# Kernel optimization log

Hardware: AMD Instinct MI355X
Metric: run time of the kernel (lower is better)

The kernel has to match this reference:

```python
import jax, jax.numpy as jnp
import numpy as np
from jax import lax

B, L = 2048, 2048
CIN, CONV, D, NCLS = 1, 128, 1024, 1000
E, H, K = 6, 2 * 1024, 2  # num_experts, expert hidden, top-k


def setup_inputs() -> dict:
    key = jax.random.key(0)
    ks = jax.random.split(key, 16)
    s = lambda *sh: 0.02
    return {
        "x": jax.random.normal(ks[0], (B, L), jnp.float32),
        "conv1_w": jax.random.normal(ks[1], (CONV, CIN, 5), jnp.float32) * 0.1,
        "conv1_b": jnp.zeros((CONV,), jnp.float32),
        "conv2_w": jax.random.normal(ks[2], (CONV, CONV, 5), jnp.float32) * 0.05,
        "conv2_b": jnp.zeros((CONV,), jnp.float32),
        "proj_w": jax.random.normal(ks[3], (D, CONV), jnp.float32) * 0.05,
        "proj_b": jnp.zeros((D,), jnp.float32),
        "router_w": jax.random.normal(ks[4], (E, D), jnp.float32) * 0.02,
        "router_b": jnp.zeros((E,), jnp.float32),
        "exp_w1": jax.random.normal(ks[5], (E, H, D), jnp.float32) * 0.02,
        "exp_b1": jnp.zeros((E, H), jnp.float32),
        "exp_w2": jax.random.normal(ks[6], (E, D, H), jnp.float32) * 0.02,
        "exp_b2": jnp.zeros((E, D), jnp.float32),
        "cls_w": jax.random.normal(ks[7], (NCLS, D), jnp.float32) * 0.02,
        "cls_b": jnp.zeros((NCLS,), jnp.float32),
    }


def _conv1d(x, w, b):
    # x: [B, C, L]; torch Conv1d(k=5, stride=2, pad=2)
    y = lax.conv_general_dilated(x, w, window_strides=(2,), padding=[(2, 2)],
                                 dimension_numbers=("NCH", "OIH", "NCH"))
    return y + b[None, :, None]


def reference(x, conv1_w, conv1_b, conv2_w, conv2_b, proj_w, proj_b,
              router_w, router_b, exp_w1, exp_b1, exp_w2, exp_b2, cls_w, cls_b):
    h = x[:, None, :]                               # [B,1,L]
    h = jax.nn.relu(_conv1d(h, conv1_w, conv1_b))   # [B,CONV,L/2]
    h = jax.nn.relu(_conv1d(h, conv2_w, conv2_b))   # [B,CONV,L/4]
    h = h.mean(axis=-1)                             # [B,CONV]
    h = h @ proj_w.T + proj_b                       # [B,D]

    # Top-2 router
    probs = jax.nn.softmax(h @ router_w.T + router_b, axis=-1)  # [B,E]
    top_vals, top_idx = lax.top_k(probs, K)                     # [B,2]
    # per-token per-expert combine weights (exact same math as masked loop)
    combine = (jax.nn.one_hot(top_idx[:, 0], E, dtype=h.dtype) * top_vals[:, 0:1]
               + jax.nn.one_hot(top_idx[:, 1], E, dtype=h.dtype) * top_vals[:, 1:2])  # [B,E]

    # all-expert FFN, then masked combine (equivalent to gather/scatter dispatch)
    hid = jax.nn.relu(jnp.einsum("bd,ehd->beh", h, exp_w1) + exp_b1)  # [B,E,H]
    eo = jnp.einsum("beh,edh->bed", hid, exp_w2) + exp_b2             # [B,E,D]
    moe = jnp.einsum("be,bed->bd", combine, eo)                       # [B,D]

    return moe @ cls_w.T + cls_b                                      # [B,NCLS]
```

## Files before the change

### kernel.cpp

```cpp
#include <hip/hip_runtime.h>
#include <hip/hip_bf16.h>
#include <hip/hip_fp16.h>
#include <stdint.h>

#define BB 2048
#define LL 2048
#define CV 128
#define DD 1024
#define NC 1000
#define EE 6
#define HH 2048

typedef __bf16 bf16_t;
typedef _Float16 f16_t;
typedef __attribute__((ext_vector_type(8))) __bf16 bf16x8;
typedef __attribute__((ext_vector_type(8))) _Float16 f16x8;
typedef __attribute__((ext_vector_type(4))) _Float16 f16x4;
typedef __attribute__((ext_vector_type(4))) float f32x4;

__device__ __forceinline__ void gload_lds16(const void* g, void* l)
{
    __builtin_amdgcn_global_load_lds(
        (const __attribute__((address_space(1))) unsigned int*)g,
        (__attribute__((address_space(3))) unsigned int*)l, 16, 0, 0);
}

__global__ void k_prep_w2(const float* __restrict__ w2, bf16_t* __restrict__ wsw)
{
    int idx = blockIdx.x * 256 + threadIdx.x;
    if (idx >= 5 * 128 * 128) return;
    int kk = idx % 5;
    int t2 = idx / 5;
    int ci = t2 & 127;
    int co = t2 >> 7;
    float v = w2[idx];
    bf16_t h = (bf16_t)v;
    bf16_t l = (bf16_t)(v - (float)h);
    int cb = ci >> 5, j = ci & 31;
    int t  = cb * 5 + kk;
    int si = (co * 32 + j) ^ ((co & 7) << 3);
    wsw[(size_t)t * 8192 + si]        = h;
    wsw[(size_t)t * 8192 + 4096 + si] = l;
}

__global__ void k_prep_exp(const float* __restrict__ ew1, const float* __restrict__ ew2,
                           const float* __restrict__ cw,  f16_t* __restrict__ ew1h,
                           f16_t* __restrict__ ew2h, f16_t* __restrict__ clsh)
{
    const size_t n1 = (size_t)EE * HH * DD / 4;
    const size_t n2 = n1 + (size_t)EE * DD * HH / 4;
    const size_t n3 = n2 + (size_t)NC * DD / 4;
    size_t i4 = (size_t)blockIdx.x * 256 + threadIdx.x;
    if (i4 >= n3) return;
    const float* src; f16_t* dst; size_t off;
    if (i4 < n1)      { src = ew1; dst = ew1h; off = i4; }
    else if (i4 < n2) { src = ew2; dst = ew2h; off = i4 - n1; }
    else              { src = cw;  dst = clsh; off = i4 - n2; }
    float4 v = reinterpret_cast<const float4*>(src)[off];
    f16x4 r;
    r[0] = (f16_t)v.x; r[1] = (f16_t)v.y; r[2] = (f16_t)v.z; r[3] = (f16_t)v.w;
    reinterpret_cast<f16x4*>(dst)[off] = r;
}

__launch_bounds__(256, 2)
__global__ void k_conv(const float* __restrict__ x,  const float* __restrict__ w1,
                       const float* __restrict__ b1, const bf16_t* __restrict__ wsw,
                       const float* __restrict__ b2, float* __restrict__ hbar)
{
    __shared__ __align__(16) float w1s[640];
    __shared__ __align__(16) float b1s[128];
    __shared__ __align__(16) float b2s[128];
    __shared__ __align__(16) short h1s[2][260 * 32];
    __shared__ __align__(16) short wlds[2][8192];

    const int tid  = threadIdx.x;
    const int b    = blockIdx.x;
    const int lane = tid & 63;
    const int wid  = tid >> 6;
    const int l15  = lane & 15, lg = lane >> 4;
    const int wm   = wid >> 1,  wn = wid & 1;
    const int jo   = tid & 3;
    const int rg   = tid >> 2;

    short* wflat = &wlds[0][0];

    for (int i = tid; i < 640; i += 256) w1s[i] = w1[i];
    if (tid < 128) { b1s[tid] = b1[tid]; b2s[tid] = b2[tid]; }

    {
        const bf16_t* src = wsw + (size_t)(wid * 4) * 512 + lane * 8;
        short* dst = wflat + (wid * 4) * 512;
#pragma unroll
        for (int o = 0; o < 4; ++o)
            gload_lds16(src + o * 512, dst + o * 512);
    }
    __syncthreads();

    const float* xrow = x + (size_t)b * LL;

    float racc[4][4];
#pragma unroll
    for (int m = 0; m < 4; ++m)
#pragma unroll
        for (int r = 0; r < 4; ++r) racc[m][r] = 0.f;

    for (int c = 0; c < 4; ++c) {
        const int t1base = 256 * c - 2;

        f32x4 acc[4][4];
#pragma unroll
        for (int m = 0; m < 4; ++m)
#pragma unroll
            for (int n = 0; n < 4; ++n)
#pragma unroll
                for (int r = 0; r < 4; ++r) acc[m][n][r] = 0.f;

        for (int cb = 0; cb < 4; ++cb) {
            const int ci0 = cb * 32 + jo * 8;
            float wf[40], br8[8];
#pragma unroll
            for (int q = 0; q < 10; ++q)
                *reinterpret_cast<float4*>(&wf[q * 4]) =
                    *reinterpret_cast<const float4*>(&w1s[ci0 * 5 + q * 4]);
            *reinterpret_cast<float4*>(&br8[0]) = *reinterpret_cast<const float4*>(&b1s[ci0]);
            *reinterpret_cast<float4*>(&br8[4]) = *reinterpret_cast<const float4*>(&b1s[ci0 + 4]);

#pragma unroll
            for (int it = 0; it < 5; ++it) {
                int r = rg + it * 64;
                if (it < 4 || r < 260) {
                    int t1 = t1base + r;
                    bool valid = (unsigned)t1 < 1024u;
                    float xv[5];
#pragma unroll
                    for (int kk = 0; kk < 5; ++kk) {
                        int xg = 2 * t1 - 2 + kk;
                        xv[kk] = (valid && (unsigned)xg < 2048u) ? xrow[xg] : 0.f;
                    }
                    bf16x8 hv, lv;
#pragma unroll
                    for (int u = 0; u < 8; ++u) {
                        float v = 0.f;
                        if (valid) {
                            v = br8[u];
#pragma unroll
                            for (int kk = 0; kk < 5; ++kk) v += wf[u * 5 + kk] * xv[kk];
                            v = fmaxf(v, 0.f);
                        }
                        bf16_t h = (bf16_t)v;
                        hv[u] = h;
                        lv[u] = (bf16_t)(v - (float)h);
                    }
                    int si = (r * 32 + jo * 8) ^ (((r >> 1) & 7) << 3);
                    *reinterpret_cast<bf16x8*>(&h1s[0][si]) = hv;
                    *reinterpret_cast<bf16x8*>(&h1s[1][si]) = lv;
                }
            }
            __syncthreads();

            for (int k = 0; k < 5; ++k) {
                const int t  = cb * 5 + k;
                const int tn = (t + 1) % 20;
                {
                    const bf16_t* src = wsw + (size_t)tn * 8192 + (wid * 4) * 512 + lane * 8;
                    short* dst = wflat + (tn & 1) * 8192 + (wid * 4) * 512;
#pragma unroll
                    for (int o = 0; o < 4; ++o)
                        gload_lds16(src + o * 512, dst + o * 512);
                }
                const short* wp = wflat + (t & 1) * 8192;
                bf16x8 ah[4], al[4];
#pragma unroll
                for (int m = 0; m < 4; ++m) {
                    int co_l = wm * 64 + m * 16 + l15;
                    int si = (co_l * 32 + lg * 8) ^ ((l15 & 7) << 3);
                    ah[m] = *reinterpret_cast<const bf16x8*>(wp + si);
                    al[m] = *reinterpret_cast<const bf16x8*>(wp + 4096 + si);
                }
                bf16x8 bh[4], bl[4];
#pragma unroll
                for (int n = 0; n < 4; ++n) {
                    int r = 2 * (wn * 64 + n * 16 + l15) + k;
                    int si = (r * 32 + lg * 8) ^ (((r >> 1) & 7) << 3);
                    bh[n] = *reinterpret_cast<const bf16x8*>(&h1s[0][si]);
                    bl[n] = *reinterpret_cast<const bf16x8*>(&h1s[1][si]);
                }
#pragma unroll
                for (int m = 0; m < 4; ++m)
#pragma unroll
                    for (int n = 0; n < 4; ++n) {
                        acc[m][n] = __builtin_amdgcn_mfma_f32_16x16x32_bf16(ah[m], bh[n], acc[m][n], 0, 0, 0);
                        acc[m][n] = __builtin_amdgcn_mfma_f32_16x16x32_bf16(ah[m], bl[n], acc[m][n], 0, 0, 0);
                        acc[m][n] = __builtin_amdgcn_mfma_f32_16x16x32_bf16(al[m], bh[n], acc[m][n], 0, 0, 0);
                    }
                __syncthreads();
            }
        }
#pragma unroll
        for (int m = 0; m < 4; ++m)
#pragma unroll
            for (int r = 0; r < 4; ++r) {
                int co = wm * 64 + m * 16 + lg * 4 + r;
                float bias = b2s[co];
                float s = 0.f;
#pragma unroll
                for (int n = 0; n < 4; ++n) s += fmaxf(acc[m][n][r] + bias, 0.f);
                racc[m][r] += s;
            }
    }

    asm volatile("s_waitcnt vmcnt(0)" ::: "memory");
    __syncthreads();

#pragma unroll
    for (int m = 0; m < 4; ++m)
#pragma unroll
        for (int r = 0; r < 4; ++r) {
            float v = racc[m][r];
            v += __shfl_xor(v, 1);
            v += __shfl_xor(v, 2);
            v += __shfl_xor(v, 4);
            v += __shfl_xor(v, 8);
            racc[m][r] = v;
        }
    float* red = (float*)wflat;
    if (l15 == 0) {
#pragma unroll
        for (int m = 0; m < 4; ++m)
#pragma unroll
            for (int r = 0; r < 4; ++r)
                red[wid * 64 + m * 16 + lg * 4 + r] = racc[m][r];
    }
    __syncthreads();
    if (tid < 128) {
        int wm2 = tid >> 6, loc = tid & 63;
        float s = red[(wm2 * 2 + 0) * 64 + loc] + red[(wm2 * 2 + 1) * 64 + loc];
        hbar[(size_t)b * 128 + tid] = s * (1.f / 512.f);
    }
}

__launch_bounds__(256)
__global__ void k_proj(const float* __restrict__ hbar, const float* __restrict__ pw,
                       const float* __restrict__ pb, float* __restrict__ h)
{
    __shared__ float hbs[64 * 128];
    const int tid = threadIdx.x;
    const int b0 = blockIdx.x * 64, d0 = blockIdx.y * 64;
    for (int i = tid * 4; i < 64 * 128; i += 1024)
        *reinterpret_cast<float4*>(&hbs[i]) =
            *reinterpret_cast<const float4*>(&hbar[(size_t)b0 * 128 + i]);
    __syncthreads();
    const int tx = tid & 15, ty = tid >> 4;
    float acc[4][4];
#pragma unroll
    for (int i = 0; i < 4; ++i)
#pragma unroll
        for (int j = 0; j < 4; ++j) acc[i][j] = 0.f;
    const float* pwr[4];
#pragma unroll
    for (int j = 0; j < 4; ++j) pwr[j] = pw + (size_t)(d0 + tx * 4 + j) * 128;
    for (int k = 0; k < 128; k += 4) {
        float4 wv[4], av[4];
#pragma unroll
        for (int j = 0; j < 4; ++j) wv[j] = *reinterpret_cast<const float4*>(pwr[j] + k);
#pragma unroll
        for (int i = 0; i < 4; ++i) av[i] = *reinterpret_cast<const float4*>(&hbs[(ty * 4 + i) * 128 + k]);
#pragma unroll
        for (int i = 0; i < 4; ++i)
#pragma unroll
            for (int j = 0; j < 4; ++j)
                acc[i][j] += av[i].x * wv[j].x + av[i].y * wv[j].y +
                             av[i].z * wv[j].z + av[i].w * wv[j].w;
    }
#pragma unroll
    for (int i = 0; i < 4; ++i) {
        int bb = b0 + ty * 4 + i;
#pragma unroll
        for (int j = 0; j < 4; ++j) {
            int d = d0 + tx * 4 + j;
            h[(size_t)bb * DD + d] = acc[i][j] + pb[d];
        }
    }
}

__launch_bounds__(256)
__global__ void k_router(const float* __restrict__ h, const float* __restrict__ rw,
                         const float* __restrict__ rb, float* __restrict__ comb,
                         int2* __restrict__ top)
{
    const int lane = threadIdx.x & 63;
    const int b = blockIdx.x * 4 + (threadIdx.x >> 6);
    float part[6] = {0.f, 0.f, 0.f, 0.f, 0.f, 0.f};
    for (int j = 0; j < 16; ++j) {
        int d = j * 64 + lane;
        float hv = h[(size_t)b * DD + d];
#pragma unroll
        for (int e = 0; e < 6; ++e) part[e] += rw[e * DD + d] * hv;
    }
#pragma unroll
    for (int e = 0; e < 6; ++e) {
        float v = part[e];
        for (int off = 32; off > 0; off >>= 1) v += __shfl_xor(v, off);
        part[e] = v;
    }
    if (lane == 0) {
        float lgt[6];
#pragma unroll
        for (int e = 0; e < 6; ++e) lgt[e] = part[e] + rb[e];
        int i1 = 0;
#pragma unroll
        for (int e = 1; e < 6; ++e) if (lgt[e] > lgt[i1]) i1 = e;
        int i2 = -1;
#pragma unroll
        for (int e = 0; e < 6; ++e)
            if (e != i1 && (i2 < 0 || lgt[e] > lgt[i2])) i2 = e;
        float mx = lgt[i1], s = 0.f, ex[6];
#pragma unroll
        for (int e = 0; e < 6; ++e) { ex[e] = expf(lgt[e] - mx); s += ex[e]; }
        float inv = 1.f / s;
#pragma unroll
        for (int e = 0; e < 6; ++e) comb[b * 8 + e] = 0.f;
        comb[b * 8 + 6] = 0.f; comb[b * 8 + 7] = 0.f;
        comb[b * 8 + i1] = ex[i1] * inv;
        comb[b * 8 + i2] = ex[i2] * inv;
        top[b] = make_int2(i1, i2);
    }
}

__global__ void k_index(const int2* __restrict__ top, int* __restrict__ meta,
                        int* __restrict__ idxg)
{
    __shared__ int wsum[4];
    const int tid = threadIdx.x, lane = tid & 63, wid = tid >> 6;
    int2 tk[8];
#pragma unroll
    for (int j = 0; j < 8; ++j) tk[j] = top[tid * 8 + j];
    int off_run = 0;
    for (int e = 0; e < 6; ++e) {
        int m[8], c = 0;
#pragma unroll
        for (int j = 0; j < 8; ++j) { m[j] = (tk[j].x == e || tk[j].y == e) ? 1 : 0; c += m[j]; }
        int v = c;
        for (int d = 1; d < 64; d <<= 1) { int u = __shfl_up(v, d); if (lane >= d) v += u; }
        if (lane == 63) wsum[wid] = v;
        __syncthreads();
        int wbase = 0;
#pragma unroll
        for (int w = 0; w < 4; ++w) if (w < wid) wbase += wsum[w];
        int total = wsum[0] + wsum[1] + wsum[2] + wsum[3];
        int p = off_run + wbase + (v - c);
#pragma unroll
        for (int j = 0; j < 8; ++j) if (m[j]) idxg[p++] = tid * 8 + j;
        if (tid == 0) { meta[e] = total; meta[8 + e] = off_run; }
        off_run += total;
        __syncthreads();
    }
    if (tid == 0) meta[14] = off_run;
}

__device__ inline f16x8 cvt8(const float4 a, const float4 b)
{
    f16x8 r;
    r[0] = (f16_t)a.x; r[1] = (f16_t)a.y; r[2] = (f16_t)a.z; r[3] = (f16_t)a.w;
    r[4] = (f16_t)b.x; r[5] = (f16_t)b.y; r[6] = (f16_t)b.z; r[7] = (f16_t)b.w;
    return r;
}

template<int EPI, int NFRAG>
__launch_bounds__(256, 3)
__global__ void k_moe(const float* __restrict__ hsrc, const f16_t* __restrict__ hidg,
                      const f16_t* __restrict__ eog, const float* __restrict__ Bp,
                      const f16_t* __restrict__ Bh, const float* __restrict__ bias,
                      f16_t* __restrict__ outH, f16_t* __restrict__ eogW,
                      float* __restrict__ outF, const float* __restrict__ comb,
                      const int2* __restrict__ top, const int* __restrict__ meta,
                      const int* __restrict__ idxg, int N, int K, int NCLIP)
{
    constexpr int BN = NFRAG * 32;
    __shared__ f16_t As[128 * 72];
    __shared__ f16_t Bs[BN * 72];
    const int tid = threadIdx.x;
    const int e  = blockIdx.z;
    const int m0 = blockIdx.x * 128, n0 = blockIdx.y * BN;
    int cnt = 1 << 30, off = 0;
    if (EPI != 3) {
        cnt = meta[e]; off = meta[8 + e];
        if (m0 >= cnt) return;
    }
    const int lane = tid & 63, wid = tid >> 6;
    const int l15 = lane & 15, lg = lane >> 4;
    const int wm = wid >> 1, wn = wid & 1;

    f32x4 acc[4][NFRAG];
#pragma unroll
    for (int i = 0; i < 4; ++i)
#pragma unroll
        for (int j = 0; j < NFRAG; ++j)
#pragma unroll
            for (int r = 0; r < 4; ++r) acc[i][j][r] = 0.f;

    for (int k0 = 0; k0 < K; k0 += 64) {
        __syncthreads();
        {
            const int row = tid >> 1, c0 = (tid & 1) * 32;
            f16x8* d = reinterpret_cast<f16x8*>(As + row * 72 + c0);
            if (EPI == 1) {
                int lr = m0 + row;
                int token = (lr < cnt) ? idxg[off + lr] : 0;
                const float4* s = reinterpret_cast<const float4*>(hsrc + (size_t)token * K + k0 + c0);
#pragma unroll
                for (int j = 0; j < 4; ++j) d[j] = cvt8(s[2 * j], s[2 * j + 1]);
            } else if (EPI == 2) {
                const uint4* s = reinterpret_cast<const uint4*>(hidg + (size_t)(off + m0 + row) * K + k0 + c0);
#pragma unroll
                for (int j = 0; j < 4; ++j) reinterpret_cast<uint4*>(d)[j] = s[j];
            } else {
                int r = m0 + row;
                const f16x8* s0 = reinterpret_cast<const f16x8*>(eog + ((size_t)r * 2) * K + k0 + c0);
                const f16x8* s1 = reinterpret_cast<const f16x8*>(eog + ((size_t)r * 2 + 1) * K + k0 + c0);
#pragma unroll
                for (int j = 0; j < 4; ++j) d[j] = s0[j] + s1[j];
            }
        }
        {
            constexpr int PERTHR = BN * 64 / 256;
            constexpr int TPR = 64 / PERTHR;
            const int row = tid / TPR, c0 = (tid % TPR) * PERTHR;
            const bool ok = (n0 + row) < NCLIP;
            f16x8* d = reinterpret_cast<f16x8*>(Bs + row * 72 + c0);
            if (Bh) {
                const uint4* s = reinterpret_cast<const uint4*>(
                    Bh + (size_t)e * N * K + (size_t)(n0 + row) * K + k0 + c0);
#pragma unroll
                for (int j = 0; j < PERTHR / 8; ++j) {
                    uint4 v = ok ? s[j] : make_uint4(0, 0, 0, 0);
                    reinterpret_cast<uint4*>(d)[j] = v;
                }
            } else {
                const float4* s = reinterpret_cast<const float4*>(
                    Bp + (size_t)e * N * K + (size_t)(n0 + row) * K + k0 + c0);
#pragma unroll
                for (int j = 0; j < PERTHR / 8; ++j) {
                    float4 a = ok ? s[2 * j]     : make_float4(0.f, 0.f, 0.f, 0.f);
                    float4 b = ok ? s[2 * j + 1] : make_float4(0.f, 0.f, 0.f, 0.f);
                    d[j] = cvt8(a, b);
                }
            }
        }
        __syncthreads();
#pragma unroll
        for (int kk = 0; kk < 64; kk += 32) {
            f16x8 af[4], bq[NFRAG];
#pragma unroll
            for (int i = 0; i < 4; ++i)
                af[i] = *reinterpret_cast<const f16x8*>(As + (wm * 64 + i * 16 + l15) * 72 + kk + lg * 8);
#pragma unroll
            for (int j = 0; j < NFRAG; ++j)
                bq[j] = *reinterpret_cast<const f16x8*>(Bs + (wn * (BN / 2) + j * 16 + l15) * 72 + kk + lg * 8);
#pragma unroll
            for (int i = 0; i < 4; ++i)
#pragma unroll
                for (int j = 0; j < NFRAG; ++j)
                    acc[i][j] = __builtin_amdgcn_mfma_f32_16x16x32_f16(af[i], bq[j], acc[i][j], 0, 0, 0);
        }
    }
#pragma unroll
    for (int i = 0; i < 4; ++i) {
#pragma unroll
        for (int j = 0; j < NFRAG; ++j) {
#pragma unroll
            for (int r = 0; r < 4; ++r) {
                int lr  = m0 + wm * 64 + i * 16 + lg * 4 + r;
                int col = n0 + wn * (BN / 2) + j * 16 + l15;
                float c = acc[i][j][r];
                if (EPI == 1) {
                    if (lr < cnt)
                        outH[(size_t)(off + lr) * N + col] = (f16_t)fmaxf(c + bias[(size_t)e * N + col], 0.f);
                } else if (EPI == 2) {
                    if (lr < cnt) {
                        int token = idxg[off + lr];
                        int slot = (top[token].x == e) ? 0 : 1;
                        float w = comb[token * 8 + e];
                        eogW[((size_t)token * 2 + slot) * N + col] = (f16_t)(w * (c + bias[(size_t)e * N + col]));
                    }
                } else {
                    if (col < NCLIP)
                        outF[(size_t)lr * NCLIP + col] = c + bias[col];
                }
            }
        }
    }
}

extern "C" void kernel_launch(void* const* d_in, const int* in_sizes, int n_in,
                              void* d_out, int out_size, void* d_ws, size_t ws_size,
                              hipStream_t stream)
{
    const float* x   = (const float*)d_in[0];
    const float* w1  = (const float*)d_in[1];
    const float* b1  = (const float*)d_in[2];
    const float* w2  = (const float*)d_in[3];
    const float* b2  = (const float*)d_in[4];
    const float* pw  = (const float*)d_in[5];
    const float* pb  = (const float*)d_in[6];
    const float* rw  = (const float*)d_in[7];
    const float* rb  = (const float*)d_in[8];
    const float* ew1 = (const float*)d_in[9];
    const float* eb1 = (const float*)d_in[10];
    const float* ew2 = (const float*)d_in[11];
    const float* eb2 = (const float*)d_in[12];
    const float* cw  = (const float*)d_in[13];
    const float* cb  = (const float*)d_in[14];
    float* out = (float*)d_out;

    char* ws = (char*)d_ws;
    bf16_t* wsw  = (bf16_t*)(ws + 0);
    float*  hbar = (float*)(ws + 327680);
    float*  h    = (float*)(ws + 1376256);
    f16_t*  eog  = (f16_t*)(ws + 1376256);
    float*  comb = (float*)(ws + 9764864);
    int2*   top  = (int2*)(ws + 9830400);
    int*    meta = (int*)(ws + 9846784);
    int*    idxg = (int*)(ws + 9847040);
    f16_t*  hidg = (f16_t*)(ws + 9863424);
    f16_t*  ew1h = (f16_t*)(ws + 27164928);
    f16_t*  ew2h = (f16_t*)(ws + 52330752);
    f16_t*  clsh = (f16_t*)(ws + 77496576);

    const bool f16w = ws_size >= 79593728ull;

    k_prep_w2<<<320, 256, 0, stream>>>(w2, wsw);
    if (f16w)
        k_prep_exp<<<25576, 256, 0, stream>>>(ew1, ew2, cw, ew1h, ew2h, clsh);
    k_conv<<<2048, 256, 0, stream>>>(x, w1, b1, wsw, b2, hbar);
    k_proj<<<dim3(32, 16), 256, 0, stream>>>(hbar, pw, pb, h);
    k_router<<<512, 256, 0, stream>>>(h, rw, rb, comb, top);
    k_index<<<1, 256, 0, stream>>>(top, meta, idxg);
    k_moe<1, 4><<<dim3(16, 16, 6), 256, 0, stream>>>(
        h, nullptr, nullptr, ew1, f16w ? ew1h : nullptr, eb1,
        hidg, nullptr, nullptr, comb, top, meta, idxg, HH, DD, HH);
    k_moe<2, 4><<<dim3(16, 8, 6), 256, 0, stream>>>(
        nullptr, hidg, nullptr, ew2, f16w ? ew2h : nullptr, eb2,
        nullptr, eog, nullptr, comb, top, meta, idxg, DD, HH, DD);
    k_moe<3, 2><<<dim3(16, 16, 1), 256, 0, stream>>>(
        nullptr, nullptr, eog, cw, f16w ? clsh : nullptr, cb,
        nullptr, nullptr, out, comb, top, meta, idxg, DD, DD, NC);
}
```

Measured before the change: 823.6 us.

## Process two batch rows per conv block sharing staged conv2 weights

The conv kernel now runs 512 threads covering two batch rows per block, so each conv2 weight tile loaded into LDS serves both rows. Weight staging moves from a per-k double buffer with a barrier every step to a three-slot buffer filled in two bulk loads per channel block, which cuts the number of barriers. MFMA issue is reordered into three independent passes (hi*hi, hi*lo, lo*hi) to shorten dependency chains. The cost is larger LDS use and 512-thread blocks, which may lower occupancy.

```diff
diff --git a/kernel.cpp b/kernel.cpp
--- a/kernel.cpp
+++ b/kernel.cpp
@@ -62,7 +62,7 @@
     reinterpret_cast<f16x4*>(dst)[off] = r;
 }
 
-__launch_bounds__(256, 2)
+__launch_bounds__(512, 2)
 __global__ void k_conv(const float* __restrict__ x,  const float* __restrict__ w1,
                        const float* __restrict__ b1, const bf16_t* __restrict__ wsw,
                        const float* __restrict__ b2, float* __restrict__ hbar)
@@ -70,39 +70,68 @@
     __shared__ __align__(16) float w1s[640];
     __shared__ __align__(16) float b1s[128];
     __shared__ __align__(16) float b2s[128];
-    __shared__ __align__(16) short h1s[2][260 * 32];
-    __shared__ __align__(16) short wlds[2][8192];
+    __shared__ __align__(16) float red[8][64];
+    __shared__ __align__(16) short h1s[2][2][8320];
+    __shared__ __align__(16) short wlds[3 * 8192];
 
     const int tid  = threadIdx.x;
-    const int b    = blockIdx.x;
+    const int b0   = blockIdx.x * 2;
     const int lane = tid & 63;
     const int wid  = tid >> 6;
     const int l15  = lane & 15, lg = lane >> 4;
-    const int wm   = wid >> 1,  wn = wid & 1;
-    const int jo   = tid & 3;
-    const int rg   = tid >> 2;
-
-    short* wflat = &wlds[0][0];
-
-    for (int i = tid; i < 640; i += 256) w1s[i] = w1[i];
+    const int wb   = wid >> 2;
+    const int wm   = (wid >> 1) & 1;
+    const int wn   = wid & 1;
+    const int gb   = tid >> 8;
+    const int gtid = tid & 255;
+    const int jo   = gtid & 3;
+    const int rg   = gtid >> 2;
+
+    for (int i = tid; i < 640; i += 512) w1s[i] = w1[i];
     if (tid < 128) { b1s[tid] = b1[tid]; b2s[tid] = b2[tid]; }
 
-    {
-        const bf16_t* src = wsw + (size_t)(wid * 4) * 512 + lane * 8;
-        short* dst = wflat + (wid * 4) * 512;
-#pragma unroll
-        for (int o = 0; o < 4; ++o)
-            gload_lds16(src + o * 512, dst + o * 512);
-    }
-    __syncthreads();
-
-    const float* xrow = x + (size_t)b * LL;
+    const float* xrow = x + (size_t)(b0 + gb) * LL;
+    const short* h1p  = &h1s[wb][0][0];
 
     float racc[4][4];
 #pragma unroll
     for (int m = 0; m < 4; ++m)
 #pragma unroll
         for (int r = 0; r < 4; ++r) racc[m][r] = 0.f;
+
+#define KSTEP(kk, buf)                                                          \
+    do {                                                                        \
+        const short* wp = wlds + (buf) * 8192;                                  \
+        bf16x8 ah[4], al[4], bh[4], bl[4];                                      \
+        _Pragma("unroll")                                                       \
+        for (int m = 0; m < 4; ++m) {                                           \
+            int si = ((wm * 64 + m * 16 + l15) * 32 + lg * 8) ^ ((l15 & 7) << 3); \
+            ah[m] = *reinterpret_cast<const bf16x8*>(wp + si);                  \
+            al[m] = *reinterpret_cast<const bf16x8*>(wp + 4096 + si);           \
+        }                                                                       \
+        _Pragma("unroll")                                                       \
+        for (int n = 0; n < 4; ++n) {                                           \
+            int r = 2 * (wn * 64 + n * 16 + l15) + (kk);                        \
+            int si = (r * 32 + lg * 8) ^ (((r >> 1) & 7) << 3);                 \
+            bh[n] = *reinterpret_cast<const bf16x8*>(h1p + si);                 \
+            bl[n] = *reinterpret_cast<const bf16x8*>(h1p + 8320 + si);          \
+        }                                                                       \
+        _Pragma("unroll")                                                       \
+        for (int m = 0; m < 4; ++m)                                             \
+            _Pragma("unroll")                                                   \
+            for (int n = 0; n < 4; ++n)                                         \
+                acc[m][n] = __builtin_amdgcn_mfma_f32_16x16x32_bf16(ah[m], bh[n], acc[m][n], 0, 0, 0); \
+        _Pragma("unroll")                                                       \
+        for (int m = 0; m < 4; ++m)                                             \
+            _Pragma("unroll")                                                   \
+            for (int n = 0; n < 4; ++n)                                         \
+                acc[m][n] = __builtin_amdgcn_mfma_f32_16x16x32_bf16(ah[m], bl[n], acc[m][n], 0, 0, 0); \
+        _Pragma("unroll")                                                       \
+        for (int m = 0; m < 4; ++m)                                             \
+            _Pragma("unroll")                                                   \
+            for (int n = 0; n < 4; ++n)                                         \
+                acc[m][n] = __builtin_amdgcn_mfma_f32_16x16x32_bf16(al[m], bh[n], acc[m][n], 0, 0, 0); \
+    } while (0)
 
     for (int c = 0; c < 4; ++c) {
         const int t1base = 256 * c - 2;
@@ -116,6 +145,17 @@
                 for (int r = 0; r < 4; ++r) acc[m][n][r] = 0.f;
 
         for (int cb = 0; cb < 4; ++cb) {
+            __syncthreads();
+
+            {
+                const bf16_t* src = wsw + (size_t)cb * 40960;
+#pragma unroll
+                for (int j = 0; j < 6; ++j) {
+                    int q = j * 512 + tid;
+                    gload_lds16(src + q * 8, wlds + q * 8);
+                }
+            }
+
             const int ci0 = cb * 32 + jo * 8;
             float wf[40], br8[8];
 #pragma unroll
@@ -152,49 +192,29 @@
                         lv[u] = (bf16_t)(v - (float)h);
                     }
                     int si = (r * 32 + jo * 8) ^ (((r >> 1) & 7) << 3);
-                    *reinterpret_cast<bf16x8*>(&h1s[0][si]) = hv;
-                    *reinterpret_cast<bf16x8*>(&h1s[1][si]) = lv;
+                    *reinterpret_cast<bf16x8*>(&h1s[gb][0][si]) = hv;
+                    *reinterpret_cast<bf16x8*>(&h1s[gb][1][si]) = lv;
                 }
             }
             __syncthreads();
 
-            for (int k = 0; k < 5; ++k) {
-                const int t  = cb * 5 + k;
-                const int tn = (t + 1) % 20;
-                {
-                    const bf16_t* src = wsw + (size_t)tn * 8192 + (wid * 4) * 512 + lane * 8;
-                    short* dst = wflat + (tn & 1) * 8192 + (wid * 4) * 512;
-#pragma unroll
-                    for (int o = 0; o < 4; ++o)
-                        gload_lds16(src + o * 512, dst + o * 512);
+            KSTEP(0, 0);
+            KSTEP(1, 1);
+            __syncthreads();
+
+            {
+                const bf16_t* src = wsw + (size_t)cb * 40960 + 24576;
+#pragma unroll
+                for (int j = 0; j < 4; ++j) {
+                    int q = j * 512 + tid;
+                    gload_lds16(src + q * 8, wlds + q * 8);
                 }
-                const short* wp = wflat + (t & 1) * 8192;
-                bf16x8 ah[4], al[4];
-#pragma unroll
-                for (int m = 0; m < 4; ++m) {
-                    int co_l = wm * 64 + m * 16 + l15;
-                    int si = (co_l * 32 + lg * 8) ^ ((l15 & 7) << 3);
-                    ah[m] = *reinterpret_cast<const bf16x8*>(wp + si);
-                    al[m] = *reinterpret_cast<const bf16x8*>(wp + 4096 + si);
-                }
-                bf16x8 bh[4], bl[4];
-#pragma unroll
-                for (int n = 0; n < 4; ++n) {
-                    int r = 2 * (wn * 64 + n * 16 + l15) + k;
-                    int si = (r * 32 + lg * 8) ^ (((r >> 1) & 7) << 3);
-                    bh[n] = *reinterpret_cast<const bf16x8*>(&h1s[0][si]);
-                    bl[n] = *reinterpret_cast<const bf16x8*>(&h1s[1][si]);
-                }
-#pragma unroll
-                for (int m = 0; m < 4; ++m)
-#pragma unroll
-                    for (int n = 0; n < 4; ++n) {
-                        acc[m][n] = __builtin_amdgcn_mfma_f32_16x16x32_bf16(ah[m], bh[n], acc[m][n], 0, 0, 0);
-                        acc[m][n] = __builtin_amdgcn_mfma_f32_16x16x32_bf16(ah[m], bl[n], acc[m][n], 0, 0, 0);
-                        acc[m][n] = __builtin_amdgcn_mfma_f32_16x16x32_bf16(al[m], bh[n], acc[m][n], 0, 0, 0);
-                    }
-                __syncthreads();
-            }
+            }
+            KSTEP(2, 2);
+            __syncthreads();
+
+            KSTEP(3, 0);
+            KSTEP(4, 1);
         }
 #pragma unroll
         for (int m = 0; m < 4; ++m)
@@ -208,9 +228,7 @@
                 racc[m][r] += s;
             }
     }
-
-    asm volatile("s_waitcnt vmcnt(0)" ::: "memory");
-    __syncthreads();
+#undef KSTEP
 
 #pragma unroll
     for (int m = 0; m < 4; ++m)
@@ -223,19 +241,19 @@
             v += __shfl_xor(v, 8);
             racc[m][r] = v;
         }
-    float* red = (float*)wflat;
     if (l15 == 0) {
 #pragma unroll
         for (int m = 0; m < 4; ++m)
 #pragma unroll
             for (int r = 0; r < 4; ++r)
-                red[wid * 64 + m * 16 + lg * 4 + r] = racc[m][r];
+                red[wid][m * 16 + lg * 4 + r] = racc[m][r];
     }
     __syncthreads();
-    if (tid < 128) {
-        int wm2 = tid >> 6, loc = tid & 63;
-        float s = red[(wm2 * 2 + 0) * 64 + loc] + red[(wm2 * 2 + 1) * 64 + loc];
-        hbar[(size_t)b * 128 + tid] = s * (1.f / 512.f);
+    if (tid < 256) {
+        int wb2 = tid >> 7, cc = tid & 127;
+        int wm2 = cc >> 6, loc = cc & 63;
+        float s = red[wb2 * 4 + wm2 * 2 + 0][loc] + red[wb2 * 4 + wm2 * 2 + 1][loc];
+        hbar[(size_t)(b0 + wb2) * 128 + cc] = s * (1.f / 512.f);
     }
 }
 
@@ -532,7 +550,7 @@
     k_prep_w2<<<320, 256, 0, stream>>>(w2, wsw);
     if (f16w)
         k_prep_exp<<<25576, 256, 0, stream>>>(ew1, ew2, cw, ew1h, ew2h, clsh);
-    k_conv<<<2048, 256, 0, stream>>>(x, w1, b1, wsw, b2, hbar);
+    k_conv<<<1024, 512, 0, stream>>>(x, w1, b1, wsw, b2, hbar);
     k_proj<<<dim3(32, 16), 256, 0, stream>>>(hbar, pw, pb, h);
     k_router<<<512, 256, 0, stream>>>(h, rw, rb, comb, top);
     k_index<<<1, 256, 0, stream>>>(top, meta, idxg);
```

Result: faster. 731.1 us (-11.2%).
